# Kernel tuning notes

Measured on AMD Instinct MI355X. Metric: run time of the kernel, lower is better.

## Reference

```python
import jax, jax.numpy as jnp
import numpy as np

N_NODES = 100000
IN_CH = 256
OUT_CH = 128
HEADS = 1
N_EDGES = 1600000
NEG_SLOPE = 0.2
EPS = 1e-16


def setup_inputs() -> dict:
    key = jax.random.key(0)
    ks = jax.random.split(key, 6)
    x = jax.random.normal(ks[0], (N_NODES, IN_CH), dtype=jnp.float32)
    edge_index = jax.random.randint(ks[1], (2, N_EDGES), 0, N_NODES, dtype=jnp.int64)
    # xavier-ish scaled params
    lin_src = jax.random.normal(ks[2], (IN_CH, OUT_CH), dtype=jnp.float32) * (1.414 * (2.0 / (IN_CH + OUT_CH)) ** 0.5)
    att_src = jax.random.normal(ks[3], (1, HEADS, OUT_CH), dtype=jnp.float32) * 0.1
    att_dst = jax.random.normal(ks[4], (1, HEADS, OUT_CH), dtype=jnp.float32) * 0.1
    bias = jnp.zeros((HEADS * OUT_CH,), dtype=jnp.float32)
    return {"x": x, "edge_index": edge_index, "lin_src": lin_src,
            "att_src": att_src, "att_dst": att_dst, "bias": bias}


def reference(x, edge_index, lin_src, att_src, att_dst, bias):
    N = x.shape[0]
    # shared projection (lin_dst is lin_src when in_channels is an int)
    xp = (x @ lin_src).reshape(N, HEADS, OUT_CH)  # [N, H, C]

    # add_self_loops: drop existing self-edges (via mask) and append N loop edges
    src, dst = edge_index[0], edge_index[1]
    loop = jnp.arange(N, dtype=edge_index.dtype)
    src_all = jnp.concatenate([src, loop])
    dst_all = jnp.concatenate([dst, loop])
    valid = jnp.concatenate([src != dst, jnp.ones((N,), dtype=bool)])  # [E+N]

    # per-node attention logits
    alpha_src = jnp.sum(xp * att_src, axis=-1)  # [N, H]
    alpha_dst = jnp.sum(xp * att_dst, axis=-1)  # [N, H]
    alpha = alpha_src[src_all] + alpha_dst[dst_all]  # [E+N, H]
    alpha = jax.nn.leaky_relu(alpha, NEG_SLOPE)

    # scatter softmax over incoming edges of each dst node (global-max stabilized,
    # matching the original src.max() over all retained edges)
    amax = jnp.max(jnp.where(valid[:, None], alpha, -jnp.inf))
    ex = jnp.exp(alpha - amax) * valid[:, None].astype(alpha.dtype)
    denom = jax.ops.segment_sum(ex, dst_all, num_segments=N)  # [N, H]
    alpha = ex / (denom[dst_all] + EPS)  # [E+N, H]

    # weighted aggregation
    weighted = xp[src_all] * alpha[..., None]  # [E+N, H, C]
    out = jax.ops.segment_sum(weighted, dst_all, num_segments=N)  # [N, H, C]

    out = out.reshape(N, HEADS * OUT_CH) + bias  # concat=True
    return out
```

## Files before the change

kernel.cpp:

```cpp
#include <hip/hip_runtime.h>
#include <cstdint>
#include <cstddef>

#define IN_CH 256
#define OUT_CH 128
#define NEG_SLOPE 0.2f
#define EPS 1e-16f

typedef __attribute__((ext_vector_type(8))) short bf16x8;
typedef __attribute__((ext_vector_type(4))) float f32x4;

__device__ __forceinline__ unsigned short f2bf(float f) {
    unsigned int u = __float_as_uint(f);
    return (unsigned short)((u + 0x7fffu + ((u >> 16) & 1u)) >> 16);
}

__global__ __launch_bounds__(256) void convert_w_kernel(const float* __restrict__ w,
                                                        unsigned short* __restrict__ wt)
{
    const int n = blockIdx.x;
    const int k = threadIdx.x;
    wt[(size_t)n * IN_CH + k] = f2bf(w[(size_t)k * OUT_CH + n]);
}

__device__ __forceinline__ void gemm_body(
    int bid, const float* __restrict__ x, const unsigned short* __restrict__ wt,
    const float* __restrict__ att_s, const float* __restrict__ att_d,
    unsigned short* __restrict__ xpb, float* __restrict__ asrc, float* __restrict__ adst,
    int M)
{
    const int tid  = threadIdx.x;
    const int wv   = tid >> 6;
    const int lane = tid & 63;
    const int lm   = lane & 15;
    const int quad = lane >> 4;
    const int arow = bid * 64 + wv * 16 + lm;
    const bool av  = arow < M;
    const float* xrow = x + (size_t)arow * IN_CH + quad * 8;

    f32x4 acc[8];
#pragma unroll
    for (int t = 0; t < 8; ++t) acc[t] = (f32x4){0.f, 0.f, 0.f, 0.f};

#pragma unroll
    for (int kk = 0; kk < 8; ++kk) {
        const int k0 = kk * 32;
        bf16x8 af = {0, 0, 0, 0, 0, 0, 0, 0};
        if (av) {
            float4 a0 = *(const float4*)(xrow + k0);
            float4 a1 = *(const float4*)(xrow + k0 + 4);
            af[0] = (short)f2bf(a0.x); af[1] = (short)f2bf(a0.y);
            af[2] = (short)f2bf(a0.z); af[3] = (short)f2bf(a0.w);
            af[4] = (short)f2bf(a1.x); af[5] = (short)f2bf(a1.y);
            af[6] = (short)f2bf(a1.z); af[7] = (short)f2bf(a1.w);
        }
#pragma unroll
        for (int t = 0; t < 8; ++t) {
            bf16x8 bf = *(const bf16x8*)(wt + (size_t)(16 * t + lm) * IN_CH + k0 + quad * 8);
            acc[t] = __builtin_amdgcn_mfma_f32_16x16x32_bf16(af, bf, acc[t], 0, 0, 0);
        }
    }

    float asw[8], adw[8];
#pragma unroll
    for (int t = 0; t < 8; ++t) {
        asw[t] = att_s[16 * t + lm];
        adw[t] = att_d[16 * t + lm];
    }
#pragma unroll
    for (int r = 0; r < 4; ++r) {
        const int orow = bid * 64 + wv * 16 + quad * 4 + r;
        if (orow < M) {
            float ps = 0.f, pd = 0.f;
            unsigned short* xr = xpb + (size_t)orow * OUT_CH + lm;
#pragma unroll
            for (int t = 0; t < 8; ++t) {
                float v = acc[t][r];
                xr[16 * t] = f2bf(v);
                ps += v * asw[t];
                pd += v * adw[t];
            }
#pragma unroll
            for (int m = 1; m < 16; m <<= 1) {
                ps += __shfl_xor(ps, m, 16);
                pd += __shfl_xor(pd, m, 16);
            }
            if (lm == 0) { asrc[orow] = ps; adst[orow] = pd; }
        }
    }
}

__device__ __forceinline__ void hist_body(
    int bid, int nblk,
    const int* __restrict__ src, const int* __restrict__ dst,
    int* __restrict__ deg, int* __restrict__ pw, int E)
{
    const int T = nblk * 256;
    const int e0 = bid * 256 + threadIdx.x;
#pragma unroll
    for (int k = 0; k < 8; ++k) {
        const int e = e0 + k * T;
        if (e < E) {
            int s = src[e], d = dst[e];
            if (s != d) pw[e] = atomicAdd(&deg[d], 1);
        }
    }
}

__global__ __launch_bounds__(256) void fused_gemm_hist_kernel(
    const float* __restrict__ x, const unsigned short* __restrict__ wt,
    const float* __restrict__ att_s, const float* __restrict__ att_d,
    unsigned short* __restrict__ xpb, float* __restrict__ asrc, float* __restrict__ adst,
    int M,
    const int* __restrict__ src, const int* __restrict__ dst,
    int* __restrict__ deg, int* __restrict__ pw, int E,
    int hist_blocks)
{
    if ((int)blockIdx.x < hist_blocks)
        hist_body(blockIdx.x, hist_blocks, src, dst, deg, pw, E);
    else
        gemm_body(blockIdx.x - hist_blocks, x, wt, att_s, att_d, xpb, asrc, adst, M);
}

#define SCAN_NB 256
#define SCAN_NT 256

__global__ __launch_bounds__(SCAN_NT) void scan_partial_kernel(
    const int* __restrict__ deg, int* __restrict__ bsum, int N)
{
    __shared__ int sh[SCAN_NT];
    const int chunk = (N + SCAN_NB - 1) / SCAN_NB;
    const int sub   = (chunk + SCAN_NT - 1) / SCAN_NT;
    const int b0 = blockIdx.x * chunk;
    const int t0 = b0 + threadIdx.x * sub;
    const int t1 = min(min(b0 + chunk, t0 + sub), N);
    int s = 0;
    for (int i = t0; i < t1; ++i) s += deg[i];
    sh[threadIdx.x] = s;
    __syncthreads();
    for (int off = SCAN_NT / 2; off > 0; off >>= 1) {
        if (threadIdx.x < off) sh[threadIdx.x] += sh[threadIdx.x + off];
        __syncthreads();
    }
    if (threadIdx.x == 0) bsum[blockIdx.x] = sh[0];
}

__global__ __launch_bounds__(SCAN_NB) void scan_blocksums_kernel(
    const int* __restrict__ bsum, int* __restrict__ boff,
    int* __restrict__ row_ptr, int N)
{
    __shared__ int sh[SCAN_NB];
    const int t = threadIdx.x;
    sh[t] = bsum[t];
    __syncthreads();
    for (int off = 1; off < SCAN_NB; off <<= 1) {
        int v = (t >= off) ? sh[t - off] : 0;
        __syncthreads();
        sh[t] += v;
        __syncthreads();
    }
    boff[t] = (t == 0) ? 0 : sh[t - 1];
    if (t == SCAN_NB - 1) row_ptr[N] = sh[t];
}

__global__ __launch_bounds__(SCAN_NT) void scan_fill_kernel(
    const int* __restrict__ deg, const int* __restrict__ boff,
    int* __restrict__ row_ptr, int N)
{
    __shared__ int sh[SCAN_NT];
    const int chunk = (N + SCAN_NB - 1) / SCAN_NB;
    const int sub   = (chunk + SCAN_NT - 1) / SCAN_NT;
    const int b0 = blockIdx.x * chunk;
    const int t0 = b0 + threadIdx.x * sub;
    const int t1 = min(min(b0 + chunk, t0 + sub), N);
    int s = 0;
    for (int i = t0; i < t1; ++i) s += deg[i];
    sh[threadIdx.x] = s;
    __syncthreads();
    for (int off = 1; off < SCAN_NT; off <<= 1) {
        int v = (threadIdx.x >= off) ? sh[threadIdx.x - off] : 0;
        __syncthreads();
        sh[threadIdx.x] += v;
        __syncthreads();
    }
    int run = boff[blockIdx.x] + ((threadIdx.x == 0) ? 0 : sh[threadIdx.x - 1]);
    for (int i = t0; i < t1; ++i) {
        row_ptr[i] = run;
        run += deg[i];
    }
}

__global__ __launch_bounds__(256) void scatter_kernel(
    const int* __restrict__ src, const int* __restrict__ dst,
    const int* __restrict__ row_ptr, const int* __restrict__ pw,
    int* __restrict__ col, int E, int nblk)
{
    const int T = nblk * 256;
    const int e0 = blockIdx.x * 256 + threadIdx.x;
#pragma unroll
    for (int k = 0; k < 8; ++k) {
        const int e = e0 + k * T;
        if (e < E) {
            int s = src[e], d = dst[e];
            if (s != d) col[row_ptr[d] + pw[e]] = s;
        }
    }
}

__global__ __launch_bounds__(256) void aggregate_kernel(
    const unsigned short* __restrict__ xpb, const float* __restrict__ asrc,
    const float* __restrict__ adst, const int* __restrict__ row_ptr,
    const int* __restrict__ col, const float* __restrict__ bias,
    float* __restrict__ out, int N)
{
    const int n = (int)((blockIdx.x * blockDim.x + threadIdx.x) >> 6);
    const int lane = threadIdx.x & 63;
    if (n >= N) return;
    const float a_d = adst[n];
    const unsigned int* xpw = (const unsigned int*)xpb;

    float ax0 = 0.f, ay0 = 0.f, ax1 = 0.f, ay1 = 0.f;
    float ax2 = 0.f, ay2 = 0.f, ax3 = 0.f, ay3 = 0.f;
    float den = 0.f;

    {
        float lg = asrc[n] + a_d;
        lg = (lg > 0.f) ? lg : lg * NEG_SLOPE;
        float ex = __expf(lg);
        den += ex;
        unsigned int v = xpw[(size_t)n * 64 + lane];
        ax0 += ex * __uint_as_float(v << 16);
        ay0 += ex * __uint_as_float(v & 0xffff0000u);
    }

    const int beg = row_ptr[n], end = row_ptr[n + 1];
    for (int base = beg; base < end; base += 64) {
        const int idx = base + lane;
        int s = 0; float ex = 0.f;
        if (idx < end) {
            s = col[idx];
            float lg = asrc[s] + a_d;
            lg = (lg > 0.f) ? lg : lg * NEG_SLOPE;
            ex = __expf(lg);
        }
        const int cnt = min(64, end - base);
        int j = 0;
        for (; j + 4 <= cnt; j += 4) {
            float e0 = __shfl(ex, j, 64),     e1 = __shfl(ex, j + 1, 64);
            float e2 = __shfl(ex, j + 2, 64), e3 = __shfl(ex, j + 3, 64);
            int   s0 = __shfl(s, j, 64),      s1 = __shfl(s, j + 1, 64);
            int   s2 = __shfl(s, j + 2, 64),  s3 = __shfl(s, j + 3, 64);
            unsigned int v0 = xpw[(size_t)s0 * 64 + lane];
            unsigned int v1 = xpw[(size_t)s1 * 64 + lane];
            unsigned int v2 = xpw[(size_t)s2 * 64 + lane];
            unsigned int v3 = xpw[(size_t)s3 * 64 + lane];
            den += (e0 + e1) + (e2 + e3);
            ax0 += e0 * __uint_as_float(v0 << 16);
            ay0 += e0 * __uint_as_float(v0 & 0xffff0000u);
            ax1 += e1 * __uint_as_float(v1 << 16);
            ay1 += e1 * __uint_as_float(v1 & 0xffff0000u);
            ax2 += e2 * __uint_as_float(v2 << 16);
            ay2 += e2 * __uint_as_float(v2 & 0xffff0000u);
            ax3 += e3 * __uint_as_float(v3 << 16);
            ay3 += e3 * __uint_as_float(v3 & 0xffff0000u);
        }
        for (; j < cnt; ++j) {
            float e0 = __shfl(ex, j, 64);
            int   s0 = __shfl(s, j, 64);
            unsigned int v0 = xpw[(size_t)s0 * 64 + lane];
            den += e0;
            ax0 += e0 * __uint_as_float(v0 << 16);
            ay0 += e0 * __uint_as_float(v0 & 0xffff0000u);
        }
    }

    const float inv = 1.f / (den + EPS);
    const float2 bv = ((const float2*)bias)[lane];
    float2 o;
    o.x = ((ax0 + ax1) + (ax2 + ax3)) * inv + bv.x;
    o.y = ((ay0 + ay1) + (ay2 + ay3)) * inv + bv.y;
    ((float2*)out)[(size_t)n * 64 + lane] = o;
}

extern "C" void kernel_launch(void* const* d_in, const int* in_sizes, int n_in,
                              void* d_out, int out_size, void* d_ws, size_t ws_size,
                              hipStream_t stream)
{
    const float* x     = (const float*)d_in[0];
    const int*   ei    = (const int*)d_in[1];
    const float* w     = (const float*)d_in[2];
    const float* att_s = (const float*)d_in[3];
    const float* att_d = (const float*)d_in[4];
    const float* bias  = (const float*)d_in[5];
    float* out = (float*)d_out;

    const int N = in_sizes[0] / IN_CH;
    const int E = in_sizes[1] / 2;
    const int* src = ei;
    const int* dst = ei + E;

    char* p = (char*)d_ws;
    auto take = [&](size_t bytes) { char* q = p; p += (bytes + 255) & ~size_t(255); return q; };
    unsigned short* xpb = (unsigned short*)take((size_t)N * OUT_CH * 2);
    unsigned short* wt  = (unsigned short*)take((size_t)OUT_CH * IN_CH * 2);
    float* asrc   = (float*)take((size_t)N * 4);
    float* adst   = (float*)take((size_t)N * 4);
    int*   deg    = (int*)take((size_t)N * 4);
    int*   row_ptr= (int*)take((size_t)(N + 1) * 4);
    int*   bsum   = (int*)take(SCAN_NB * 4);
    int*   boff   = (int*)take(SCAN_NB * 4);
    int*   pw     = (int*)take((size_t)E * 4);
    int*   col    = (int*)take((size_t)E * 4);

    hipMemsetAsync(deg, 0, (size_t)N * 4, stream);
    convert_w_kernel<<<OUT_CH, IN_CH, 0, stream>>>(w, wt);

    const int gemm_blocks = (N + 63) / 64;
    const int hist_blocks = (E + 256 * 8 - 1) / (256 * 8);
    fused_gemm_hist_kernel<<<hist_blocks + gemm_blocks, 256, 0, stream>>>(
        x, wt, att_s, att_d, xpb, asrc, adst, N,
        src, dst, deg, pw, E, hist_blocks);

    scan_partial_kernel<<<SCAN_NB, SCAN_NT, 0, stream>>>(deg, bsum, N);
    scan_blocksums_kernel<<<1, SCAN_NB, 0, stream>>>(bsum, boff, row_ptr, N);
    scan_fill_kernel<<<SCAN_NB, SCAN_NT, 0, stream>>>(deg, boff, row_ptr, N);

    const int sc_blocks = (E + 256 * 8 - 1) / (256 * 8);
    scatter_kernel<<<sc_blocks, 256, 0, stream>>>(src, dst, row_ptr, pw, col, E, sc_blocks);

    aggregate_kernel<<<(N + 3) / 4, 256, 0, stream>>>(
        xpb, asrc, adst, row_ptr, col, bias, out, N);
}
```

Before: 382.4 us.

## Privatize degree histogram per XCD with workgroup-scope atomics

The in-degree histogram is split into one private copy per XCD, chosen from the hardware XCC id register. Increments use relaxed workgroup-scope atomics, so they no longer need device-wide coherence. Each edge's slot is packed as XCD id plus local position; the scan sums the copies and turns each into per-XCD offsets, which the scatter uses to place columns. Histogram blocks also handle fewer edges each, and the trade is an 8x larger memset and scan read plus reliance on atomics to the same address staying coherent within one XCD.

```diff
diff --git a/kernel.cpp b/kernel.cpp
--- a/kernel.cpp
+++ b/kernel.cpp
@@ -6,6 +6,9 @@
 #define OUT_CH 128
 #define NEG_SLOPE 0.2f
 #define EPS 1e-16f
+
+#define NXCD 8
+#define XCC_ID_HWREG 6164
 
 typedef __attribute__((ext_vector_type(8))) short bf16x8;
 typedef __attribute__((ext_vector_type(4))) float f32x4;
@@ -93,16 +96,23 @@
 __device__ __forceinline__ void hist_body(
     int bid, int nblk,
     const int* __restrict__ src, const int* __restrict__ dst,
-    int* __restrict__ deg, int* __restrict__ pw, int E)
-{
+    int* __restrict__ deg_part, int N, int* __restrict__ pw, int E)
+{
+    const int xcd = (int)(__builtin_amdgcn_s_getreg(XCC_ID_HWREG) & 7u);
+    int* mydeg = deg_part + (size_t)xcd * N;
     const int T = nblk * 256;
     const int e0 = bid * 256 + threadIdx.x;
 #pragma unroll
-    for (int k = 0; k < 8; ++k) {
+    for (int k = 0; k < 2; ++k) {
         const int e = e0 + k * T;
         if (e < E) {
             int s = src[e], d = dst[e];
-            if (s != d) pw[e] = atomicAdd(&deg[d], 1);
+            if (s != d) {
+                int pos = __hip_atomic_fetch_add(&mydeg[d], 1,
+                                                 __ATOMIC_RELAXED,
+                                                 __HIP_MEMORY_SCOPE_WORKGROUP);
+                pw[e] = (xcd << 27) | pos;
+            }
         }
     }
 }
@@ -113,11 +123,11 @@
     unsigned short* __restrict__ xpb, float* __restrict__ asrc, float* __restrict__ adst,
     int M,
     const int* __restrict__ src, const int* __restrict__ dst,
-    int* __restrict__ deg, int* __restrict__ pw, int E,
+    int* __restrict__ deg_part, int* __restrict__ pw, int E,
     int hist_blocks)
 {
     if ((int)blockIdx.x < hist_blocks)
-        hist_body(blockIdx.x, hist_blocks, src, dst, deg, pw, E);
+        hist_body(blockIdx.x, hist_blocks, src, dst, deg_part, M, pw, E);
     else
         gemm_body(blockIdx.x - hist_blocks, x, wt, att_s, att_d, xpb, asrc, adst, M);
 }
@@ -126,7 +136,7 @@
 #define SCAN_NT 256
 
 __global__ __launch_bounds__(SCAN_NT) void scan_partial_kernel(
-    const int* __restrict__ deg, int* __restrict__ bsum, int N)
+    const int* __restrict__ deg_part, int* __restrict__ bsum, int N)
 {
     __shared__ int sh[SCAN_NT];
     const int chunk = (N + SCAN_NB - 1) / SCAN_NB;
@@ -135,7 +145,10 @@
     const int t0 = b0 + threadIdx.x * sub;
     const int t1 = min(min(b0 + chunk, t0 + sub), N);
     int s = 0;
-    for (int i = t0; i < t1; ++i) s += deg[i];
+    for (int i = t0; i < t1; ++i) {
+#pragma unroll
+        for (int xx = 0; xx < NXCD; ++xx) s += deg_part[(size_t)xx * N + i];
+    }
     sh[threadIdx.x] = s;
     __syncthreads();
     for (int off = SCAN_NT / 2; off > 0; off >>= 1) {
@@ -164,7 +177,7 @@
 }
 
 __global__ __launch_bounds__(SCAN_NT) void scan_fill_kernel(
-    const int* __restrict__ deg, const int* __restrict__ boff,
+    int* __restrict__ deg_part, const int* __restrict__ boff,
     int* __restrict__ row_ptr, int N)
 {
     __shared__ int sh[SCAN_NT];
@@ -174,7 +187,10 @@
     const int t0 = b0 + threadIdx.x * sub;
     const int t1 = min(min(b0 + chunk, t0 + sub), N);
     int s = 0;
-    for (int i = t0; i < t1; ++i) s += deg[i];
+    for (int i = t0; i < t1; ++i) {
+#pragma unroll
+        for (int xx = 0; xx < NXCD; ++xx) s += deg_part[(size_t)xx * N + i];
+    }
     sh[threadIdx.x] = s;
     __syncthreads();
     for (int off = 1; off < SCAN_NT; off <<= 1) {
@@ -186,13 +202,18 @@
     int run = boff[blockIdx.x] + ((threadIdx.x == 0) ? 0 : sh[threadIdx.x - 1]);
     for (int i = t0; i < t1; ++i) {
         row_ptr[i] = run;
-        run += deg[i];
+#pragma unroll
+        for (int xx = 0; xx < NXCD; ++xx) {
+            int c = deg_part[(size_t)xx * N + i];
+            deg_part[(size_t)xx * N + i] = run;
+            run += c;
+        }
     }
 }
 
 __global__ __launch_bounds__(256) void scatter_kernel(
     const int* __restrict__ src, const int* __restrict__ dst,
-    const int* __restrict__ row_ptr, const int* __restrict__ pw,
+    const int* __restrict__ deg_part, int N, const int* __restrict__ pw,
     int* __restrict__ col, int E, int nblk)
 {
     const int T = nblk * 256;
@@ -202,7 +223,12 @@
         const int e = e0 + k * T;
         if (e < E) {
             int s = src[e], d = dst[e];
-            if (s != d) col[row_ptr[d] + pw[e]] = s;
+            if (s != d) {
+                unsigned int p = (unsigned int)pw[e];
+                int xcd = (int)(p >> 27);
+                int pos = (int)(p & 0x07ffffffu);
+                col[deg_part[(size_t)xcd * N + d] + pos] = s;
+            }
         }
     }
 }
@@ -305,28 +331,28 @@
     unsigned short* wt  = (unsigned short*)take((size_t)OUT_CH * IN_CH * 2);
     float* asrc   = (float*)take((size_t)N * 4);
     float* adst   = (float*)take((size_t)N * 4);
-    int*   deg    = (int*)take((size_t)N * 4);
-    int*   row_ptr= (int*)take((size_t)(N + 1) * 4);
+    int*   deg_part = (int*)take((size_t)NXCD * N * 4);
+    int*   row_ptr  = (int*)take((size_t)(N + 1) * 4);
     int*   bsum   = (int*)take(SCAN_NB * 4);
     int*   boff   = (int*)take(SCAN_NB * 4);
     int*   pw     = (int*)take((size_t)E * 4);
     int*   col    = (int*)take((size_t)E * 4);
 
-    hipMemsetAsync(deg, 0, (size_t)N * 4, stream);
+    hipMemsetAsync(deg_part, 0, (size_t)NXCD * N * 4, stream);
     convert_w_kernel<<<OUT_CH, IN_CH, 0, stream>>>(w, wt);
 
     const int gemm_blocks = (N + 63) / 64;
-    const int hist_blocks = (E + 256 * 8 - 1) / (256 * 8);
+    const int hist_blocks = (E + 256 * 2 - 1) / (256 * 2);
     fused_gemm_hist_kernel<<<hist_blocks + gemm_blocks, 256, 0, stream>>>(
         x, wt, att_s, att_d, xpb, asrc, adst, N,
-        src, dst, deg, pw, E, hist_blocks);
-
-    scan_partial_kernel<<<SCAN_NB, SCAN_NT, 0, stream>>>(deg, bsum, N);
+        src, dst, deg_part, pw, E, hist_blocks);
+
+    scan_partial_kernel<<<SCAN_NB, SCAN_NT, 0, stream>>>(deg_part, bsum, N);
     scan_blocksums_kernel<<<1, SCAN_NB, 0, stream>>>(bsum, boff, row_ptr, N);
-    scan_fill_kernel<<<SCAN_NB, SCAN_NT, 0, stream>>>(deg, boff, row_ptr, N);
+    scan_fill_kernel<<<SCAN_NB, SCAN_NT, 0, stream>>>(deg_part, boff, row_ptr, N);
 
     const int sc_blocks = (E + 256 * 8 - 1) / (256 * 8);
-    scatter_kernel<<<sc_blocks, 256, 0, stream>>>(src, dst, row_ptr, pw, col, E, sc_blocks);
+    scatter_kernel<<<sc_blocks, 256, 0, stream>>>(src, dst, deg_part, N, pw, col, E, sc_blocks);
 
     aggregate_kernel<<<(N + 3) / 4, 256, 0, stream>>>(
         xpb, asrc, adst, row_ptr, col, bias, out, N);
```

Result: no change. 383.3 us (+0.3%).
